# Kernel optimization log

Measured on AMD Instinct MI355X. Metric: run time of the kernel, lower is better.

## Reference

```python
import jax, jax.numpy as jnp
import numpy as np

HIDDEN = 1024
HEADS = 16
HEAD_SIZE = HIDDEN // HEADS


def setup_inputs() -> dict:
    key = jax.random.key(0)
    k0, k1, k2, k3 = jax.random.split(key, 4)
    scale = 1.0 / np.sqrt(HIDDEN)
    return {
        "input_data": jax.random.normal(k0, (4, 4096, HIDDEN), dtype=jnp.float32),
        "W0": jax.random.normal(k1, (HIDDEN, HIDDEN), dtype=jnp.float32) * scale,
        "W1": jax.random.normal(k2, (HIDDEN, HIDDEN), dtype=jnp.float32) * scale,
        "W2": jax.random.normal(k3, (HIDDEN, HIDDEN), dtype=jnp.float32) * scale,
    }


def reference(input_data, W0, W1, W2):
    b, s, _ = input_data.shape
    k, h = HEADS, HEAD_SIZE
    # torch.nn.Linear(bias=False): y = x @ W.T
    out = input_data @ W0.T          # [b, s, hidden]
    out1 = input_data @ W1.T
    out2 = input_data @ W2.T
    # reshape to heads; cummax over the sequence axis (axis=1 here, which
    # matches cummax(dim=2) on the permuted (b,k,s,h) layout in torch)
    out_h = out.reshape(b, s, k, h)
    out1_h = out1.reshape(b, s, k, h)
    cm = jax.lax.associative_scan(jnp.maximum, (out_h + out1_h) / jnp.sqrt(jnp.float32(h)), axis=1)
    cm = cm.reshape(b, s, k * h)
    out = (cm + out2) * cm + out1
    return out
```

## Files before the change

### kernel.cpp

```cpp
#include <hip/hip_runtime.h>
#include <cstdint>
#include <cstddef>

#define HIDDEN 1024
#define BATCH 4
#define SEQ 4096
#define M_ROWS (BATCH * SEQ)
#define K_DIM 1024
#define SUBCHUNK 32
#define NSUB (SEQ / SUBCHUNK)

typedef __bf16 bf16_t;
typedef __bf16 v8bf __attribute__((ext_vector_type(8)));
typedef float v4f __attribute__((ext_vector_type(4)));

__device__ __forceinline__ unsigned short f32_to_bf16(float f) {
  unsigned int u = __float_as_uint(f);
  u += 0x7fffu + ((u >> 16) & 1u);
  return (unsigned short)(u >> 16);
}
__device__ __forceinline__ float bf16_to_f32(unsigned short u) {
  return __uint_as_float((unsigned int)u << 16);
}

__global__ void convert_kernel(const float* __restrict__ X,
                               const float* __restrict__ W0,
                               const float* __restrict__ W1,
                               const float* __restrict__ W2,
                               unsigned short* __restrict__ Xb,
                               unsigned short* __restrict__ Wb,
                               int* __restrict__ flags) {
  int bx = blockIdx.x;
  if (bx == 0 && threadIdx.x == 0) { flags[0] = 0; flags[1] = 0; }
  if (bx < 16384) {
    int i = bx * 256 + threadIdx.x;
    float4 f = ((const float4*)X)[i];
    ushort4 u;
    u.x = f32_to_bf16(f.x); u.y = f32_to_bf16(f.y);
    u.z = f32_to_bf16(f.z); u.w = f32_to_bf16(f.w);
    ((ushort4*)Xb)[i] = u;
  } else {
    int i = (bx - 16384) * 256 + threadIdx.x;
    int mat = i >> 18;
    int off = i & 0x3FFFF;
    float4 f;
    if (mat == 0) {
      float4 a = ((const float4*)W0)[off];
      float4 b = ((const float4*)W1)[off];
      f.x = (a.x + b.x) * 0.125f; f.y = (a.y + b.y) * 0.125f;
      f.z = (a.z + b.z) * 0.125f; f.w = (a.w + b.w) * 0.125f;
    } else {
      const float* src = (mat == 1) ? W1 : W2;
      f = ((const float4*)src)[off];
    }
    ushort4 u;
    u.x = f32_to_bf16(f.x); u.y = f32_to_bf16(f.y);
    u.z = f32_to_bf16(f.z); u.w = f32_to_bf16(f.w);
    ((ushort4*)Wb)[i] = u;
  }
}


__global__ __launch_bounds__(512, 2) void gemm_s_kernel(
    const bf16_t* __restrict__ A, const bf16_t* __restrict__ B,
    unsigned short* __restrict__ Lp, float* __restrict__ cmax) {
  extern __shared__ __align__(16) char smem[];

  const int tid = threadIdx.x;
  const int wave = tid >> 6;
  const int lane = tid & 63;
  const int quad = lane >> 4;
  const int r16 = lane & 15;
  const int wr = wave >> 2;
  const int wc = wave & 3;

  const int orig = (int)blockIdx.x;
  const int swz = (orig & 7) * 32 + (orig >> 3);
  const int bx = swz & 3;
  const int mt = swz >> 2;
  const int mtile0 = mt * 256;
  const int nbase = bx * 256;

  const int l3 = lane >> 3;
  const int lc = lane & 7;
  const size_t laneOff = (size_t)l3 * K_DIM + (size_t)((lc ^ l3) << 3);
  const bf16_t* Ag = A + (size_t)(mtile0 + wave * 8) * K_DIM + laneOff;
  const bf16_t* Bg = B + (size_t)(nbase + wave * 8) * K_DIM + laneOff;

  const int aRow = (wr * 128 + r16) * 128;
  const int bRow = (wc * 64 + r16) * 128;
  const int cxor = (r16 & 7) * 16;
  const int qx = quad * 16;

  v4f acc[8][4];
#pragma unroll
  for (int i = 0; i < 8; ++i)
#pragma unroll
    for (int j = 0; j < 4; ++j) acc[i][j] = (v4f)(0.0f);

  v8bf afr[4];
  v8bf bfr[4][2];

#define STG_A(d, q, kt) __builtin_amdgcn_global_load_lds( \
    (__attribute__((address_space(1))) void*)(Ag + (size_t)(q) * (64 * K_DIM) + (size_t)(kt) * 64), \
    (__attribute__((address_space(3))) void*)(smem + (d) * 32768 + (q) * 8192 + wave * 1024), 16, 0, 0)
#define STG_B(d, q, kt) __builtin_amdgcn_global_load_lds( \
    (__attribute__((address_space(1))) void*)(Bg + (size_t)(q) * (64 * K_DIM) + (size_t)(kt) * 64), \
    (__attribute__((address_space(3))) void*)(smem + 65536 + (d) * 32768 + (q) * 8192 + wave * 1024), 16, 0, 0)
#define LDA(d, i, kk) (*(const v8bf*)(smem + (d) * 32768 + aRow + (i) * 2048 + (((kk) * 64 + qx) ^ cxor)))
#define LDB(d, j, kk) (*(const v8bf*)(smem + 65536 + (d) * 32768 + bRow + (j) * 2048 + (((kk) * 64 + qx) ^ cxor)))
#define RD_A(d, ih, kk) { _Pragma("unroll") for (int ii = 0; ii < 4; ++ii) afr[ii] = LDA(d, (ih) * 4 + ii, kk); }
#define RD_B(d, kk) { _Pragma("unroll") for (int j = 0; j < 4; ++j) bfr[j][kk] = LDB(d, j, kk); }
#define MM(ih, kk) \
  __builtin_amdgcn_s_barrier(); \
  asm volatile("s_waitcnt lgkmcnt(0)" ::: "memory"); \
  __builtin_amdgcn_s_setprio(1); \
  { _Pragma("unroll") for (int ii = 0; ii < 4; ++ii) { _Pragma("unroll") for (int j = 0; j < 4; ++j) \
      acc[(ih) * 4 + ii][j] = __builtin_amdgcn_mfma_f32_16x16x32_bf16(afr[ii], bfr[j][(kk)], acc[(ih) * 4 + ii][j], 0, 0, 0); } } \
  __builtin_amdgcn_s_setprio(0);
#define BAR() __builtin_amdgcn_s_barrier()
#define WAITV(n) asm volatile("s_waitcnt vmcnt(" #n ")" ::: "memory")

  STG_A(0, 0, 0); STG_A(0, 1, 0); STG_A(0, 2, 0); STG_A(0, 3, 0);
  STG_B(0, 0, 0); STG_B(0, 1, 0); STG_B(0, 2, 0); STG_B(0, 3, 0);
  STG_A(1, 0, 1); STG_A(1, 2, 1); STG_B(1, 0, 1); STG_B(1, 1, 1);
  WAITV(4);
  BAR();

  for (int it = 0; it < 7; ++it) {
    const int t1 = 2 * it + 1, t2 = t1 + 1, t3 = t1 + 2;
    RD_A(0, 0, 0); RD_B(0, 0);
    STG_B(1, 2, t1); STG_B(1, 3, t1);
    MM(0, 0); BAR();
    RD_B(0, 1); RD_A(0, 0, 1);
    STG_A(1, 1, t1); STG_A(1, 3, t1);
    MM(0, 1); BAR();
    RD_A(0, 1, 0);
    STG_A(0, 0, t2); STG_A(0, 2, t2);
    MM(1, 0); BAR();
    RD_A(0, 1, 1);
    STG_B(0, 0, t2); STG_B(0, 1, t2);
    MM(1, 1); WAITV(4); BAR();
    RD_A(1, 0, 0); RD_B(1, 0);
    STG_B(0, 2, t2); STG_B(0, 3, t2);
    MM(0, 0); BAR();
    RD_B(1, 1); RD_A(1, 0, 1);
    STG_A(0, 1, t2); STG_A(0, 3, t2);
    MM(0, 1); BAR();
    RD_A(1, 1, 0);
    STG_A(1, 0, t3); STG_A(1, 2, t3);
    MM(1, 0); BAR();
    RD_A(1, 1, 1);
    STG_B(1, 0, t3); STG_B(1, 1, t3);
    MM(1, 1); WAITV(4); BAR();
  }
  RD_A(0, 0, 0); RD_B(0, 0);
  STG_B(1, 2, 15); STG_B(1, 3, 15);
  MM(0, 0); BAR();
  RD_B(0, 1); RD_A(0, 0, 1);
  STG_A(1, 1, 15); STG_A(1, 3, 15);
  MM(0, 1); BAR();
  RD_A(0, 1, 0); MM(1, 0); BAR();
  RD_A(0, 1, 1); MM(1, 1); WAITV(0); BAR();
  RD_A(1, 0, 0); RD_B(1, 0); MM(0, 0); BAR();
  RD_B(1, 1); RD_A(1, 0, 1); MM(0, 1); BAR();
  RD_A(1, 1, 0); MM(1, 0); BAR();
  RD_A(1, 1, 1); MM(1, 1);

#undef STG_A
#undef STG_B
#undef LDA
#undef LDB
#undef RD_A
#undef RD_B
#undef MM
#undef BAR
#undef WAITV

  const int ncol0 = bx * 256;
  const int bidx = mtile0 >> 12;
  const int sub0 = (mtile0 & 4095) >> 5;
  ushort4* Lq4 = (ushort4*)Lp;
#pragma unroll
  for (int s = 0; s < 4; ++s) {
#pragma unroll
    for (int j = 0; j < 4; ++j) {
      float c0[4], c1[4];
      c0[0] = acc[s * 2][j][0];
      c1[0] = acc[s * 2 + 1][j][0];
#pragma unroll
      for (int r = 1; r < 4; ++r) {
        c0[r] = fmaxf(c0[r - 1], acc[s * 2][j][r]);
        c1[r] = fmaxf(c1[r - 1], acc[s * 2 + 1][j][r]);
      }
      float t0 = c0[3], t1 = c1[3], u;
      u = __shfl_up(t0, 16); if (quad >= 1) t0 = fmaxf(t0, u);
      u = __shfl_up(t0, 32); if (quad >= 2) t0 = fmaxf(t0, u);
      u = __shfl_up(t1, 16); if (quad >= 1) t1 = fmaxf(t1, u);
      u = __shfl_up(t1, 32); if (quad >= 2) t1 = fmaxf(t1, u);
      float e0 = __shfl_up(t0, 16); if (quad == 0) e0 = -INFINITY;
      float e1 = __shfl_up(t1, 16); if (quad == 0) e1 = -INFINITY;
      float T0 = __shfl(t0, 48 + r16);
      float T1 = __shfl(t1, 48 + r16);
      const int gfb = mt * 8 + bx * 2 + (wc >> 1);
      const int thrC = (wr * 4 + (wc & 1) * 2 + (j >> 1)) * 64 + lane;
      ushort4 q0, q1;
      q0.x = f32_to_bf16(fmaxf(c0[0], e0));
      q0.y = f32_to_bf16(fmaxf(c0[1], e0));
      q0.z = f32_to_bf16(fmaxf(c0[2], e0));
      q0.w = f32_to_bf16(fmaxf(c0[3], e0));
      float f1 = fmaxf(e1, T0);
      q1.x = f32_to_bf16(fmaxf(c1[0], f1));
      q1.y = f32_to_bf16(fmaxf(c1[1], f1));
      q1.z = f32_to_bf16(fmaxf(c1[2], f1));
      q1.w = f32_to_bf16(fmaxf(c1[3], f1));
      Lq4[((size_t)gfb * 16 + (s * 2 + 0) * 2 + (j & 1)) * 512 + thrC] = q0;
      Lq4[((size_t)gfb * 16 + (s * 2 + 1) * 2 + (j & 1)) * 512 + thrC] = q1;
      if (quad == 0) {
        int sub = sub0 + wr * 4 + s;
        int col = ncol0 + wc * 64 + j * 16 + r16;
        cmax[((size_t)bidx * NSUB + sub) * HIDDEN + col] = fmaxf(T0, T1);
      }
    }
  }
}

__global__ __launch_bounds__(512, 2) void gemm_f_kernel(
    const bf16_t* __restrict__ A, const bf16_t* __restrict__ B,
    const unsigned short* __restrict__ Lp, const float* __restrict__ cmax,
    float* __restrict__ pmax, int* __restrict__ flags,
    float* __restrict__ out) {
  extern __shared__ __align__(16) char smem[];

  const int tid = threadIdx.x;
  const int wave = tid >> 6;
  const int lane = tid & 63;
  const int quad = lane >> 4;
  const int r16 = lane & 15;
  const int wr = wave >> 2;
  const int wc = wave & 3;

  const int orig = (int)blockIdx.x;
  const int swz = (orig & 7) * 64 + (orig >> 3);
  const int mt = swz >> 3;
  const int nt = swz & 7;
  const int mtile0 = mt * 256;
  const int ncol0 = nt * 128;

  if (wave == 0) {
    int ticket = 0;
    if (lane == 0)
      ticket = __hip_atomic_fetch_add(&flags[0], 1, __ATOMIC_RELAXED,
                                      __HIP_MEMORY_SCOPE_AGENT);
    ticket = __shfl(ticket, 0);
    if (ticket < 64) {
      const int pb = ticket >> 4;
      const int pcol = (ticket & 15) * 64 + lane;
      const float* cp = cmax + (size_t)pb * NSUB * HIDDEN + pcol;
      float* pp = pmax + (size_t)pb * NSUB * HIDDEN + pcol;
      float run = -INFINITY;
#pragma unroll 1
      for (int s0 = 0; s0 < NSUB; s0 += 16) {
        float v[16];
#pragma unroll
        for (int i = 0; i < 16; ++i) v[i] = cp[(size_t)(s0 + i) * HIDDEN];
#pragma unroll
        for (int i = 0; i < 16; ++i) {
          pp[(size_t)(s0 + i) * HIDDEN] = run;
          run = fmaxf(run, v[i]);
        }
      }
      asm volatile("s_waitcnt vmcnt(0)" ::: "memory");
      __threadfence();
      if (lane == 0)
        __hip_atomic_fetch_add(&flags[1], 1, __ATOMIC_RELEASE,
                               __HIP_MEMORY_SCOPE_AGENT);
    }
  }

  const int l3 = lane >> 3;
  const int lc = lane & 7;
  const size_t laneOff = (size_t)l3 * K_DIM + (size_t)((lc ^ l3) << 3);
  const bf16_t* Ag = A + (size_t)(mtile0 + wave * 8) * K_DIM + laneOff;
  const bf16_t* Bg1 = B + (size_t)(1024 + ncol0 + wave * 8) * K_DIM + laneOff;
  const bf16_t* Bg2 = B + (size_t)(2048 + ncol0 + wave * 8) * K_DIM + laneOff;

  const int aRow = (wr * 128 + r16) * 128;
  const int bRow = (wc * 32 + r16) * 128;
  const int cxor = (r16 & 7) * 16;
  const int qx = quad * 16;

  v4f acc1[8][2], acc2[8][2];
#pragma unroll
  for (int i = 0; i < 8; ++i)
#pragma unroll
    for (int j = 0; j < 2; ++j) { acc1[i][j] = (v4f)(0.0f); acc2[i][j] = (v4f)(0.0f); }

  v8bf afr[4];
  v8bf b1fr[2][2], b2fr[2][2];

#define STG2_A(d, q, kt) __builtin_amdgcn_global_load_lds( \
    (__attribute__((address_space(1))) void*)(Ag + (size_t)(q) * (64 * K_DIM) + (size_t)(kt) * 64), \
    (__attribute__((address_space(3))) void*)(smem + (d) * 32768 + (q) * 8192 + wave * 1024), 16, 0, 0)
#define STG2_B1(d, q, kt) __builtin_amdgcn_global_load_lds( \
    (__attribute__((address_space(1))) void*)(Bg1 + (size_t)(q) * (64 * K_DIM) + (size_t)(kt) * 64), \
    (__attribute__((address_space(3))) void*)(smem + 65536 + (d) * 32768 + (q) * 8192 + wave * 1024), 16, 0, 0)
#define STG2_B2(d, q, kt) __builtin_amdgcn_global_load_lds( \
    (__attribute__((address_space(1))) void*)(Bg2 + (size_t)(q) * (64 * K_DIM) + (size_t)(kt) * 64), \
    (__attribute__((address_space(3))) void*)(smem + 65536 + (d) * 32768 + 16384 + (q) * 8192 + wave * 1024), 16, 0, 0)
#define LDA2(d, i, kk) (*(const v8bf*)(smem + (d) * 32768 + aRow + (i) * 2048 + (((kk) * 64 + qx) ^ cxor)))
#define LDB21(d, j, kk) (*(const v8bf*)(smem + 65536 + (d) * 32768 + bRow + (j) * 2048 + (((kk) * 64 + qx) ^ cxor)))
#define LDB22(d, j, kk) (*(const v8bf*)(smem + 65536 + (d) * 32768 + 16384 + bRow + (j) * 2048 + (((kk) * 64 + qx) ^ cxor)))
#define RD2_A(d, ih, kk) { _Pragma("unroll") for (int ii = 0; ii < 4; ++ii) afr[ii] = LDA2(d, (ih) * 4 + ii, kk); }
#define RD2_B(d, kk) { _Pragma("unroll") for (int j = 0; j < 2; ++j) { b1fr[j][kk] = LDB21(d, j, kk); b2fr[j][kk] = LDB22(d, j, kk); } }
#define MM2(ih, kk) \
  __builtin_amdgcn_s_barrier(); \
  asm volatile("s_waitcnt lgkmcnt(0)" ::: "memory"); \
  __builtin_amdgcn_s_setprio(1); \
  { _Pragma("unroll") for (int ii = 0; ii < 4; ++ii) { _Pragma("unroll") for (int j = 0; j < 2; ++j) { \
      acc1[(ih) * 4 + ii][j] = __builtin_amdgcn_mfma_f32_16x16x32_bf16(afr[ii], b1fr[j][(kk)], acc1[(ih) * 4 + ii][j], 0, 0, 0); \
      acc2[(ih) * 4 + ii][j] = __builtin_amdgcn_mfma_f32_16x16x32_bf16(afr[ii], b2fr[j][(kk)], acc2[(ih) * 4 + ii][j], 0, 0, 0); } } } \
  __builtin_amdgcn_s_setprio(0);
#define BAR() __builtin_amdgcn_s_barrier()
#define WAITV(n) asm volatile("s_waitcnt vmcnt(" #n ")" ::: "memory")

  STG2_A(0, 0, 0); STG2_A(0, 1, 0); STG2_A(0, 2, 0); STG2_A(0, 3, 0);
  STG2_B1(0, 0, 0); STG2_B1(0, 1, 0); STG2_B2(0, 0, 0); STG2_B2(0, 1, 0);
  STG2_A(1, 0, 1); STG2_A(1, 2, 1); STG2_B1(1, 0, 1); STG2_B1(1, 1, 1);
  WAITV(4);
  BAR();

  for (int it = 0; it < 7; ++it) {
    const int t1 = 2 * it + 1, t2 = t1 + 1, t3 = t1 + 2;
    RD2_A(0, 0, 0); RD2_B(0, 0);
    STG2_B2(1, 0, t1); STG2_B2(1, 1, t1);
    MM2(0, 0); BAR();
    RD2_B(0, 1); RD2_A(0, 0, 1);
    STG2_A(1, 1, t1); STG2_A(1, 3, t1);
    MM2(0, 1); BAR();
    RD2_A(0, 1, 0);
    STG2_A(0, 0, t2); STG2_A(0, 2, t2);
    MM2(1, 0); BAR();
    RD2_A(0, 1, 1);
    STG2_B1(0, 0, t2); STG2_B1(0, 1, t2);
    MM2(1, 1); WAITV(4); BAR();
    RD2_A(1, 0, 0); RD2_B(1, 0);
    STG2_B2(0, 0, t2); STG2_B2(0, 1, t2);
    MM2(0, 0); BAR();
    RD2_B(1, 1); RD2_A(1, 0, 1);
    STG2_A(0, 1, t2); STG2_A(0, 3, t2);
    MM2(0, 1); BAR();
    RD2_A(1, 1, 0);
    STG2_A(1, 0, t3); STG2_A(1, 2, t3);
    MM2(1, 0); BAR();
    RD2_A(1, 1, 1);
    STG2_B1(1, 0, t3); STG2_B1(1, 1, t3);
    MM2(1, 1); WAITV(4); BAR();
  }
  RD2_A(0, 0, 0); RD2_B(0, 0);
  STG2_B2(1, 0, 15); STG2_B2(1, 1, 15);
  MM2(0, 0); BAR();
  RD2_B(0, 1); RD2_A(0, 0, 1);
  STG2_A(1, 1, 15); STG2_A(1, 3, 15);
  MM2(0, 1); BAR();
  RD2_A(0, 1, 0); MM2(1, 0); BAR();
  RD2_A(0, 1, 1); MM2(1, 1); WAITV(0); BAR();

  const int gfb = mt * 8 + nt;
  const ushort4* Lq4 = (const ushort4*)Lp;
  ushort4 lfv[8][2];
#pragma unroll
  for (int i = 0; i < 8; ++i)
#pragma unroll
    for (int j = 0; j < 2; ++j)
      lfv[i][j] = Lq4[((size_t)gfb * 16 + i * 2 + j) * 512 + tid];

  RD2_A(1, 0, 0); RD2_B(1, 0); MM2(0, 0); BAR();
  RD2_B(1, 1); RD2_A(1, 0, 1); MM2(0, 1); BAR();
  RD2_A(1, 1, 0); MM2(1, 0); BAR();
  RD2_A(1, 1, 1); MM2(1, 1);

#undef STG2_A
#undef STG2_B1
#undef STG2_B2
#undef LDA2
#undef LDB21
#undef LDB22
#undef RD2_A
#undef RD2_B
#undef MM2
#undef BAR
#undef WAITV

  if (tid == 0) {
    while (__hip_atomic_load(&flags[1], __ATOMIC_ACQUIRE,
                             __HIP_MEMORY_SCOPE_AGENT) < 64)
      __builtin_amdgcn_s_sleep(2);
  }
  __syncthreads();

  const int bidx = mtile0 >> 12;
  const int sub0 = (mtile0 & 4095) >> 5;
#pragma unroll
  for (int i = 0; i < 8; ++i) {
    const int subr = sub0 + wr * 4 + (i >> 1);
#pragma unroll
    for (int j = 0; j < 2; ++j) {
      const int col = ncol0 + wc * 32 + j * 16 + r16;
      const float pm = pmax[((size_t)bidx * NSUB + subr) * HIDDEN + col];
      const ushort4 q = lfv[i][j];
      const int row0 = mtile0 + wr * 128 + i * 16 + quad * 4;
      float m0 = fmaxf(pm, bf16_to_f32(q.x));
      float m1 = fmaxf(pm, bf16_to_f32(q.y));
      float m2 = fmaxf(pm, bf16_to_f32(q.z));
      float m3 = fmaxf(pm, bf16_to_f32(q.w));
      size_t idx = (size_t)row0 * HIDDEN + col;
      out[idx] = (m0 + acc2[i][j][0]) * m0 + acc1[i][j][0];
      out[idx + HIDDEN] = (m1 + acc2[i][j][1]) * m1 + acc1[i][j][1];
      out[idx + 2 * HIDDEN] = (m2 + acc2[i][j][2]) * m2 + acc1[i][j][2];
      out[idx + 3 * HIDDEN] = (m3 + acc2[i][j][3]) * m3 + acc1[i][j][3];
    }
  }
}

extern "C" void kernel_launch(void* const* d_in, const int* in_sizes, int n_in,
                              void* d_out, int out_size, void* d_ws, size_t ws_size,
                              hipStream_t stream) {
  const float* X = (const float*)d_in[0];
  const float* W0 = (const float*)d_in[1];
  const float* W1 = (const float*)d_in[2];
  const float* W2 = (const float*)d_in[3];
  float* out = (float*)d_out;

  char* ws = (char*)d_ws;
  unsigned short* Xb = (unsigned short*)ws;
  unsigned short* Wb = (unsigned short*)(ws + 33554432);
  unsigned short* Lp = (unsigned short*)(ws + 33554432 + 6291456);
  int* flags = (int*)(ws + 2 * 33554432 + 6291456);
  float* cmax = (float*)(ws + 4 * 33554432 + 6291456);
  float* pmax = (float*)(ws + 4 * 33554432 + 6291456 + 2097152);

  convert_kernel<<<19456, 256, 0, stream>>>(X, W0, W1, W2, Xb, Wb, flags);

  gemm_s_kernel<<<256, 512, 131072, stream>>>((const bf16_t*)Xb, (const bf16_t*)Wb,
                                              Lp, cmax);

  gemm_f_kernel<<<512, 512, 131072, stream>>>((const bf16_t*)Xb, (const bf16_t*)Wb,
                                              Lp, cmax, pmax, flags, out);
}
```

Before: 132.6 us.

## Replace global prefix-max barrier with per-slice claim and flag synchronization

The cross-subchunk prefix-max scan moves from the start of the GEMM kernel, where 64 ticketed waves did it and every block waited on a global counter, to after the GEMM main loop. Work is split into 16 slices, one per (batch, 256-column group). The first block to reach a slice computes its prefix with 256 threads, and the other blocks spin only on that slice's ready flag. This removes the all-blocks barrier, but the scan now runs after the GEMM, so it is no longer overlapped with it, and the claimant block adds serial latency. Correctness depends on cmax being fully written before the kernel starts.

Measured after the change: 182.6 us. 1.38x slower.

```diff
diff --git a/kernel.cpp b/kernel.cpp
--- a/kernel.cpp
+++ b/kernel.cpp
@@ -31,7 +31,7 @@
                                unsigned short* __restrict__ Wb,
                                int* __restrict__ flags) {
   int bx = blockIdx.x;
-  if (bx == 0 && threadIdx.x == 0) { flags[0] = 0; flags[1] = 0; }
+  if (bx == 0 && threadIdx.x < 32) flags[threadIdx.x] = 0;
   if (bx < 16384) {
     int i = bx * 256 + threadIdx.x;
     float4 f = ((const float4*)X)[i];
@@ -247,37 +247,6 @@
   const int mtile0 = mt * 256;
   const int ncol0 = nt * 128;
 
-  if (wave == 0) {
-    int ticket = 0;
-    if (lane == 0)
-      ticket = __hip_atomic_fetch_add(&flags[0], 1, __ATOMIC_RELAXED,
-                                      __HIP_MEMORY_SCOPE_AGENT);
-    ticket = __shfl(ticket, 0);
-    if (ticket < 64) {
-      const int pb = ticket >> 4;
-      const int pcol = (ticket & 15) * 64 + lane;
-      const float* cp = cmax + (size_t)pb * NSUB * HIDDEN + pcol;
-      float* pp = pmax + (size_t)pb * NSUB * HIDDEN + pcol;
-      float run = -INFINITY;
-#pragma unroll 1
-      for (int s0 = 0; s0 < NSUB; s0 += 16) {
-        float v[16];
-#pragma unroll
-        for (int i = 0; i < 16; ++i) v[i] = cp[(size_t)(s0 + i) * HIDDEN];
-#pragma unroll
-        for (int i = 0; i < 16; ++i) {
-          pp[(size_t)(s0 + i) * HIDDEN] = run;
-          run = fmaxf(run, v[i]);
-        }
-      }
-      asm volatile("s_waitcnt vmcnt(0)" ::: "memory");
-      __threadfence();
-      if (lane == 0)
-        __hip_atomic_fetch_add(&flags[1], 1, __ATOMIC_RELEASE,
-                               __HIP_MEMORY_SCOPE_AGENT);
-    }
-  }
-
   const int l3 = lane >> 3;
   const int lc = lane & 7;
   const size_t laneOff = (size_t)l3 * K_DIM + (size_t)((lc ^ l3) << 3);
@@ -392,14 +361,48 @@
 #undef BAR
 #undef WAITV
 
+  const int bidx = mtile0 >> 12;
+  const int slice = bidx * 4 + (nt >> 1);
+  volatile int* sclaim = (volatile int*)smem;
   if (tid == 0) {
-    while (__hip_atomic_load(&flags[1], __ATOMIC_ACQUIRE,
-                             __HIP_MEMORY_SCOPE_AGENT) < 64)
-      __builtin_amdgcn_s_sleep(2);
+    int old = __hip_atomic_fetch_add(&flags[slice], 1, __ATOMIC_RELAXED,
+                                     __HIP_MEMORY_SCOPE_AGENT);
+    *sclaim = (old == 0) ? 1 : 0;
   }
   __syncthreads();
-
-  const int bidx = mtile0 >> 12;
+  if (*sclaim) {
+    if (tid < 256) {
+      const int col = (nt >> 1) * 256 + tid;
+      const float* cp = cmax + (size_t)bidx * NSUB * HIDDEN + col;
+      float* pp = pmax + (size_t)bidx * NSUB * HIDDEN + col;
+      float run = -INFINITY;
+#pragma unroll 1
+      for (int s0 = 0; s0 < NSUB; s0 += 16) {
+        float v[16];
+#pragma unroll
+        for (int i = 0; i < 16; ++i) v[i] = cp[(size_t)(s0 + i) * HIDDEN];
+#pragma unroll
+        for (int i = 0; i < 16; ++i) {
+          pp[(size_t)(s0 + i) * HIDDEN] = run;
+          run = fmaxf(run, v[i]);
+        }
+      }
+    }
+    asm volatile("s_waitcnt vmcnt(0)" ::: "memory");
+    __threadfence();
+    __syncthreads();
+    if (tid == 0)
+      __hip_atomic_store(&flags[16 + slice], 1, __ATOMIC_RELEASE,
+                         __HIP_MEMORY_SCOPE_AGENT);
+  } else {
+    if (tid == 0) {
+      while (__hip_atomic_load(&flags[16 + slice], __ATOMIC_ACQUIRE,
+                               __HIP_MEMORY_SCOPE_AGENT) == 0)
+        __builtin_amdgcn_s_sleep(2);
+    }
+    __syncthreads();
+  }
+
   const int sub0 = (mtile0 & 4095) >> 5;
 #pragma unroll
   for (int i = 0; i < 8; ++i) {
```
